# Kernel tuning notes

Hardware: AMD Instinct MI355X
Metric: run time of the kernel (lower is better)

## Reference

```python
import jax, jax.numpy as jnp
import numpy as np

B, S, ENC, DEC, ATTN = 32, 4096, 512, 512, 512


def setup_inputs() -> dict:
    key = jax.random.key(0)
    k1, k2, k3, k4, k5, k6 = jax.random.split(key, 6)
    h = jax.random.normal(k1, (B, DEC), dtype=jnp.float32)
    enc_out = jax.random.normal(k2, (B, S, ENC), dtype=jnp.float32)
    mask = jax.random.randint(k3, (B, S), 0, 2).astype(bool)
    # torch nn.Linear(in, out, bias=False): y = x @ W.T with W [out, in].
    # Store weights as [in, out] so y = x @ W; same math.
    sc = 1.0 / np.sqrt(DEC)
    W_h = jax.random.normal(k4, (DEC, ATTN), dtype=jnp.float32) * sc
    W_s = jax.random.normal(k5, (ENC, ATTN), dtype=jnp.float32) * sc
    v = jax.random.normal(k6, (ATTN,), dtype=jnp.float32) * sc
    return {"h": h, "enc_out": enc_out, "mask": mask, "W_h": W_h, "W_s": W_s, "v": v}


def reference(h, enc_out, mask, W_h, W_s, v):
    # query: [B, 1, A]; key: [B, S, A]
    query = (h @ W_h)[:, None, :]
    key = jnp.einsum("bse,ea->bsa", enc_out, W_s)
    energy = jnp.tanh(query + key)                    # [B, S, A]
    score = jnp.einsum("bsa,a->bs", energy, v)        # v^T tanh(...)
    score = jnp.where(mask, jnp.float32(-1e9), score)
    attn = jax.nn.softmax(score, axis=-1)             # [B, S]
    ctx = jnp.einsum("bs,bse->be", attn, enc_out)     # weighted sum
    return (ctx, attn)
```

## Files before the change

kernel.cpp:

```cpp
#include <hip/hip_runtime.h>
#include <hip/hip_bf16.h>
#include <math.h>

#define BB 32
#define SS 4096
#define EE 512
#define AA 512

typedef short bf16x8 __attribute__((ext_vector_type(8)));
typedef float f32x4 __attribute__((ext_vector_type(4)));
typedef unsigned short u16x4 __attribute__((ext_vector_type(4)));

__device__ __forceinline__ unsigned short f2bf(float f) {
  unsigned int u = __float_as_uint(f);
  u += 0x7fffu + ((u >> 16) & 1u);
  return (unsigned short)(u >> 16);
}

__device__ __forceinline__ float bf2f(unsigned short s) {
  return __uint_as_float(((unsigned int)s) << 16);
}

__device__ __forceinline__ float tanh_fast(float x) {
  return 1.f - 2.f / (__expf(2.f * x) + 1.f);
}

__global__ void query_kernel(const float* __restrict__ h,
                             const float* __restrict__ Wh,
                             float* __restrict__ q) {
  __shared__ float hrow[EE];
  int b = blockIdx.x;
  int t = threadIdx.x;
  for (int i = t; i < EE; i += 256) hrow[i] = h[b * EE + i];
  __syncthreads();
  float a0 = 0.f, a1 = 0.f;
  for (int e = 0; e < EE; ++e) {
    float hv = hrow[e];
    a0 += hv * Wh[e * AA + t];
    a1 += hv * Wh[e * AA + t + 256];
  }
  q[b * AA + t] = a0;
  q[b * AA + t + 256] = a1;
}

__global__ void wst_kernel(const float* __restrict__ Ws,
                           unsigned short* __restrict__ Wst) {
  int i = blockIdx.x * 256 + threadIdx.x;
  int a = i >> 9, e = i & 511;
  Wst[a * EE + e] = f2bf(Ws[e * AA + a]);
}

__global__ __launch_bounds__(256, 2) void fused_kernel(
    const float* __restrict__ enc, const unsigned short* __restrict__ Wst,
    const float* __restrict__ q, const float* __restrict__ v,
    const int* __restrict__ mask,
    float* __restrict__ rawscore,
    float* __restrict__ ctxp,
    float* __restrict__ mbuf) {
  __shared__ __align__(16) unsigned short Atile[64 * 512];
  __shared__ float spart[4][64];
  __shared__ float wrow[64];
  __shared__ float pbuf[4][512];
  const int b = blockIdx.y, chunk = blockIdx.x;
  const int s0 = chunk * 64;
  const int tid = threadIdx.x;

  const float4* src = (const float4*)(enc + ((size_t)b * SS + s0) * EE);
  for (int pass = 0; pass < 2; ++pass) {
#pragma unroll
    for (int i = 0; i < 16; ++i) {
      int idx = (pass * 16 + i) * 256 + tid;
      float4 x = src[idx];
      int row = idx >> 7;
      int c4 = idx & 127;
      int ch = c4 >> 1;
      int within = (c4 & 1) * 4;
      int cs = ch ^ (row & 7);
      u16x4 p;
      p.x = f2bf(x.x); p.y = f2bf(x.y); p.z = f2bf(x.z); p.w = f2bf(x.w);
      *(u16x4*)&Atile[row * 512 + cs * 8 + within] = p;
    }
  }
  __syncthreads();

  const int w = tid >> 6, lane = tid & 63;
  const int quad = lane >> 4, l16 = lane & 15;

  float srow[4][4];
#pragma unroll
  for (int m = 0; m < 4; ++m)
#pragma unroll
    for (int r = 0; r < 4; ++r) srow[m][r] = 0.f;

  for (int h = 0; h < 2; ++h) {
    const int n0 = w * 128 + h * 64;
    f32x4 acc[4][4];
#pragma unroll
    for (int m = 0; m < 4; ++m)
#pragma unroll
      for (int n = 0; n < 4; ++n) acc[m][n] = (f32x4){0.f, 0.f, 0.f, 0.f};

    const unsigned short* wb = Wst + (size_t)(n0 + l16) * EE + quad * 8;
#pragma unroll 2
    for (int k0 = 0; k0 < 512; k0 += 32) {
      int cs = ((k0 >> 3) + quad) ^ (l16 & 7);
      bf16x8 aF[4], bF[4];
#pragma unroll
      for (int m = 0; m < 4; ++m)
        aF[m] = *(const bf16x8*)&Atile[(m * 16 + l16) * 512 + cs * 8];
#pragma unroll
      for (int n = 0; n < 4; ++n)
        bF[n] = *(const bf16x8*)&wb[(size_t)n * 16 * EE + k0];
#pragma unroll
      for (int m = 0; m < 4; ++m)
#pragma unroll
        for (int n = 0; n < 4; ++n)
          acc[m][n] =
              __builtin_amdgcn_mfma_f32_16x16x32_bf16(aF[m], bF[n], acc[m][n], 0, 0, 0);
    }
#pragma unroll
    for (int n = 0; n < 4; ++n) {
      float qn = q[b * AA + n0 + n * 16 + l16];
      float vn = v[n0 + n * 16 + l16];
#pragma unroll
      for (int m = 0; m < 4; ++m)
#pragma unroll
        for (int r = 0; r < 4; ++r)
          srow[m][r] += tanh_fast(qn + acc[m][n][r]) * vn;
    }
  }

#pragma unroll
  for (int m = 0; m < 4; ++m)
#pragma unroll
    for (int r = 0; r < 4; ++r) {
      float s = srow[m][r];
      s += __shfl_xor(s, 1, 64);
      s += __shfl_xor(s, 2, 64);
      s += __shfl_xor(s, 4, 64);
      s += __shfl_xor(s, 8, 64);
      if (l16 == 0) spart[w][m * 16 + quad * 4 + r] = s;
    }
  __syncthreads();

  if (tid < 64) {
    float raw = spart[0][tid] + spart[1][tid] + spart[2][tid] + spart[3][tid];
    float sc = mask[(size_t)b * SS + s0 + tid] ? -1e9f : raw;
    rawscore[(size_t)b * SS + s0 + tid] = sc;
    float mx = sc;
    for (int off = 1; off < 64; off <<= 1)
      mx = fmaxf(mx, __shfl_xor(mx, off, 64));
    wrow[tid] = __expf(sc - mx);
    if (tid == 0) mbuf[b * 64 + chunk] = mx;
  }
  __syncthreads();

  {
    const int c = tid & 63;
    const int sg = tid >> 6;
    float a8[8] = {0.f, 0.f, 0.f, 0.f, 0.f, 0.f, 0.f, 0.f};
#pragma unroll
    for (int i = 0; i < 16; ++i) {
      int row = sg * 16 + i;
      float wgt = wrow[row];
      bf16x8 av = *(const bf16x8*)&Atile[row * 512 + ((c ^ (row & 7)) * 8)];
#pragma unroll
      for (int j = 0; j < 8; ++j)
        a8[j] += wgt * bf2f((unsigned short)av[j]);
    }
#pragma unroll
    for (int j = 0; j < 8; ++j) pbuf[sg][c * 8 + j] = a8[j];
  }
  __syncthreads();
#pragma unroll
  for (int jj = 0; jj < 2; ++jj) {
    int e = jj * 256 + tid;
    ctxp[((size_t)b * 64 + chunk) * EE + e] =
        pbuf[0][e] + pbuf[1][e] + pbuf[2][e] + pbuf[3][e];
  }
}

__global__ void finalize_kernel(float* __restrict__ attn,
                                const float* __restrict__ ctxp,
                                const float* __restrict__ mbuf,
                                float* __restrict__ ctx) {
  __shared__ float red[8];
  __shared__ float fc[64];
  int b = blockIdx.x, t = threadIdx.x;
  float* row = attn + (size_t)b * SS;
  float vals[16];
  float m = -3e38f;
#pragma unroll
  for (int i = 0; i < 16; ++i) {
    float x = row[i * 256 + t];
    vals[i] = x;
    m = fmaxf(m, x);
  }
  for (int off = 1; off < 64; off <<= 1) m = fmaxf(m, __shfl_xor(m, off, 64));
  int wv = t >> 6, ln = t & 63;
  if (ln == 0) red[wv] = m;
  __syncthreads();
  m = fmaxf(fmaxf(red[0], red[1]), fmaxf(red[2], red[3]));
  float sum = 0.f;
#pragma unroll
  for (int i = 0; i < 16; ++i) { vals[i] = __expf(vals[i] - m); sum += vals[i]; }
  for (int off = 1; off < 64; off <<= 1) sum += __shfl_xor(sum, off, 64);
  if (ln == 0) red[4 + wv] = sum;
  __syncthreads();
  sum = red[4] + red[5] + red[6] + red[7];
  float inv = 1.f / sum;
#pragma unroll
  for (int i = 0; i < 16; ++i) row[i * 256 + t] = vals[i] * inv;

  if (t < 64) fc[t] = __expf(mbuf[b * 64 + t] - m) * inv;
  __syncthreads();
#pragma unroll
  for (int jj = 0; jj < 2; ++jj) {
    int e = jj * 256 + t;
    const float* p = ctxp + (size_t)b * 64 * EE + e;
    float s = 0.f;
#pragma unroll
    for (int c = 0; c < 64; ++c) s += fc[c] * p[c * EE];
    ctx[b * EE + e] = s;
  }
}

extern "C" void kernel_launch(void* const* d_in, const int* in_sizes, int n_in,
                              void* d_out, int out_size, void* d_ws, size_t ws_size,
                              hipStream_t stream) {
  const float* h    = (const float*)d_in[0];
  const float* enc  = (const float*)d_in[1];
  const int*   mask = (const int*)d_in[2];
  const float* Wh   = (const float*)d_in[3];
  const float* Ws   = (const float*)d_in[4];
  const float* v    = (const float*)d_in[5];

  float* out  = (float*)d_out;
  float* ctx  = out;
  float* attn = out + BB * EE;

  char* ws = (char*)d_ws;
  float* qws = (float*)ws;                         ws += (size_t)BB * AA * 4;
  unsigned short* Wst = (unsigned short*)ws;       ws += (size_t)AA * EE * 2;
  float* ctxp = (float*)ws;                        ws += (size_t)BB * 64 * EE * 4;
  float* mbuf = (float*)ws;

  hipLaunchKernelGGL(query_kernel, dim3(32), dim3(256), 0, stream, h, Wh, qws);
  hipLaunchKernelGGL(wst_kernel, dim3(1024), dim3(256), 0, stream, Ws, Wst);
  hipLaunchKernelGGL(fused_kernel, dim3(SS / 64, BB), dim3(256), 0, stream,
                     enc, Wst, qws, v, mask, attn, ctxp, mbuf);
  hipLaunchKernelGGL(finalize_kernel, dim3(BB), dim3(256), 0, stream,
                     attn, ctxp, mbuf, ctx);
}
```

Before: 540.9 us.

## Pipeline encoder tile loads with MFMA, widen blocks to 512 threads, tile Ws transpose

The fused kernel now uses 512 threads, with each wave owning 64 attention columns. It streams the encoder tile in eight 64-column chunks, using register double buffering so global loads overlap MFMA work on the chunk already staged. The ctx partial reduction becomes one thread per feature with no pbuf scratch. The Ws transpose uses a shared-memory tile for coalesced access, and finalize moves to 512 threads. The trade-offs are a barrier per chunk, more register pressure from the 4-blocks-per-CU launch bound, and a 64KB LDS tile that may limit how many blocks actually fit per CU.

Measured after the change: 529.9 us. 1.02x faster.

```diff
diff --git a/kernel.cpp b/kernel.cpp
--- a/kernel.cpp
+++ b/kernel.cpp
@@ -45,12 +45,24 @@
 
 __global__ void wst_kernel(const float* __restrict__ Ws,
                            unsigned short* __restrict__ Wst) {
-  int i = blockIdx.x * 256 + threadIdx.x;
-  int a = i >> 9, e = i & 511;
-  Wst[a * EE + e] = f2bf(Ws[e * AA + a]);
-}
-
-__global__ __launch_bounds__(256, 2) void fused_kernel(
+  __shared__ unsigned short tile[64][65];
+  const int a0 = blockIdx.x * 64, e0 = blockIdx.y * 64;
+  const int t = threadIdx.x;
+  const int c = t & 63, r0 = t >> 6;
+#pragma unroll
+  for (int i = 0; i < 16; ++i) {
+    int e = r0 + i * 4;
+    tile[c][e] = f2bf(Ws[(size_t)(e0 + e) * AA + a0 + c]);
+  }
+  __syncthreads();
+#pragma unroll
+  for (int i = 0; i < 16; ++i) {
+    int a = r0 + i * 4;
+    Wst[(size_t)(a0 + a) * EE + e0 + c] = tile[a][c];
+  }
+}
+
+__global__ __launch_bounds__(512, 4) void fused_kernel(
     const float* __restrict__ enc, const unsigned short* __restrict__ Wst,
     const float* __restrict__ q, const float* __restrict__ v,
     const int* __restrict__ mask,
@@ -58,78 +70,91 @@
     float* __restrict__ ctxp,
     float* __restrict__ mbuf) {
   __shared__ __align__(16) unsigned short Atile[64 * 512];
-  __shared__ float spart[4][64];
+  __shared__ float spart[8][64];
   __shared__ float wrow[64];
-  __shared__ float pbuf[4][512];
   const int b = blockIdx.y, chunk = blockIdx.x;
   const int s0 = chunk * 64;
   const int tid = threadIdx.x;
-
-  const float4* src = (const float4*)(enc + ((size_t)b * SS + s0) * EE);
-  for (int pass = 0; pass < 2; ++pass) {
-#pragma unroll
-    for (int i = 0; i < 16; ++i) {
-      int idx = (pass * 16 + i) * 256 + tid;
-      float4 x = src[idx];
-      int row = idx >> 7;
-      int c4 = idx & 127;
-      int ch = c4 >> 1;
-      int within = (c4 & 1) * 4;
-      int cs = ch ^ (row & 7);
+  const int w = tid >> 6, lane = tid & 63;
+  const int quad = lane >> 4, l16 = lane & 15;
+  const int n0 = w * 64;
+
+  const int rbase = tid >> 4;
+  const int c4 = tid & 15;
+  const int sw3 = (rbase & 7) << 3;
+  const float4* src4 = (const float4*)(enc + ((size_t)b * SS + s0) * EE);
+  const float4* g0 = src4 + rbase * 128 + c4;
+  const float4* g1 = g0 + 32 * 128;
+  unsigned short* st0 = &Atile[rbase * 512 + ((c4 * 4) ^ sw3)];
+  unsigned short* st1 = st0 + 32 * 512;
+
+  const unsigned short* wb = Wst + (size_t)(n0 + l16) * EE + quad * 8;
+
+  f32x4 acc[4][4];
+#pragma unroll
+  for (int m = 0; m < 4; ++m)
+#pragma unroll
+    for (int j = 0; j < 4; ++j) acc[m][j] = (f32x4){0.f, 0.f, 0.f, 0.f};
+
+  float4 rb[2][2];
+  rb[0][0] = g0[0];
+  rb[0][1] = g1[0];
+
+#pragma unroll
+  for (int c = 0; c < 8; ++c) {
+    const int cur = c & 1, nxt = cur ^ 1;
+    {
+      float4 x = rb[cur][0];
       u16x4 p;
       p.x = f2bf(x.x); p.y = f2bf(x.y); p.z = f2bf(x.z); p.w = f2bf(x.w);
-      *(u16x4*)&Atile[row * 512 + cs * 8 + within] = p;
-    }
-  }
-  __syncthreads();
-
-  const int w = tid >> 6, lane = tid & 63;
-  const int quad = lane >> 4, l16 = lane & 15;
+      *(u16x4*)(st0 + c * 64) = p;
+      float4 y = rb[cur][1];
+      u16x4 p2;
+      p2.x = f2bf(y.x); p2.y = f2bf(y.y); p2.z = f2bf(y.z); p2.w = f2bf(y.w);
+      *(u16x4*)(st1 + c * 64) = p2;
+    }
+    if (c < 7) {
+      rb[nxt][0] = g0[(c + 1) * 16];
+      rb[nxt][1] = g1[(c + 1) * 16];
+    }
+    asm volatile("s_waitcnt lgkmcnt(0)" ::: "memory");
+    __builtin_amdgcn_s_barrier();
+#pragma unroll
+    for (int kk = 0; kk < 2; ++kk) {
+      const int k0 = c * 64 + kk * 32;
+      bf16x8 aF[4];
+#pragma unroll
+      for (int m = 0; m < 4; ++m) {
+        const int row = m * 16 + l16;
+        aF[m] = *(const bf16x8*)&Atile[row * 512 +
+                                       ((k0 + quad * 8) ^ ((row & 7) << 3))];
+      }
+#pragma unroll
+      for (int j = 0; j < 4; ++j) {
+        bf16x8 bF = *(const bf16x8*)&wb[(size_t)j * 16 * EE + k0];
+#pragma unroll
+        for (int m = 0; m < 4; ++m)
+          acc[m][j] = __builtin_amdgcn_mfma_f32_16x16x32_bf16(aF[m], bF,
+                                                              acc[m][j], 0, 0, 0);
+      }
+    }
+  }
 
   float srow[4][4];
 #pragma unroll
   for (int m = 0; m < 4; ++m)
 #pragma unroll
     for (int r = 0; r < 4; ++r) srow[m][r] = 0.f;
-
-  for (int h = 0; h < 2; ++h) {
-    const int n0 = w * 128 + h * 64;
-    f32x4 acc[4][4];
+#pragma unroll
+  for (int j = 0; j < 4; ++j) {
+    float qn = q[b * AA + n0 + j * 16 + l16];
+    float vn = v[n0 + j * 16 + l16];
 #pragma unroll
     for (int m = 0; m < 4; ++m)
 #pragma unroll
-      for (int n = 0; n < 4; ++n) acc[m][n] = (f32x4){0.f, 0.f, 0.f, 0.f};
-
-    const unsigned short* wb = Wst + (size_t)(n0 + l16) * EE + quad * 8;
-#pragma unroll 2
-    for (int k0 = 0; k0 < 512; k0 += 32) {
-      int cs = ((k0 >> 3) + quad) ^ (l16 & 7);
-      bf16x8 aF[4], bF[4];
-#pragma unroll
-      for (int m = 0; m < 4; ++m)
-        aF[m] = *(const bf16x8*)&Atile[(m * 16 + l16) * 512 + cs * 8];
-#pragma unroll
-      for (int n = 0; n < 4; ++n)
-        bF[n] = *(const bf16x8*)&wb[(size_t)n * 16 * EE + k0];
-#pragma unroll
-      for (int m = 0; m < 4; ++m)
-#pragma unroll
-        for (int n = 0; n < 4; ++n)
-          acc[m][n] =
-              __builtin_amdgcn_mfma_f32_16x16x32_bf16(aF[m], bF[n], acc[m][n], 0, 0, 0);
-    }
-#pragma unroll
-    for (int n = 0; n < 4; ++n) {
-      float qn = q[b * AA + n0 + n * 16 + l16];
-      float vn = v[n0 + n * 16 + l16];
-#pragma unroll
-      for (int m = 0; m < 4; ++m)
-#pragma unroll
-        for (int r = 0; r < 4; ++r)
-          srow[m][r] += tanh_fast(qn + acc[m][n][r]) * vn;
-    }
-  }
-
+      for (int r = 0; r < 4; ++r)
+        srow[m][r] += tanh_fast(qn + acc[m][j][r]) * vn;
+  }
 #pragma unroll
   for (int m = 0; m < 4; ++m)
 #pragma unroll
@@ -144,7 +169,9 @@
   __syncthreads();
 
   if (tid < 64) {
-    float raw = spart[0][tid] + spart[1][tid] + spart[2][tid] + spart[3][tid];
+    float raw = 0.f;
+#pragma unroll
+    for (int ww = 0; ww < 8; ++ww) raw += spart[ww][tid];
     float sc = mask[(size_t)b * SS + s0 + tid] ? -1e9f : raw;
     rawscore[(size_t)b * SS + s0 + tid] = sc;
     float mx = sc;
@@ -156,43 +183,27 @@
   __syncthreads();
 
   {
-    const int c = tid & 63;
-    const int sg = tid >> 6;
-    float a8[8] = {0.f, 0.f, 0.f, 0.f, 0.f, 0.f, 0.f, 0.f};
-#pragma unroll
-    for (int i = 0; i < 16; ++i) {
-      int row = sg * 16 + i;
-      float wgt = wrow[row];
-      bf16x8 av = *(const bf16x8*)&Atile[row * 512 + ((c ^ (row & 7)) * 8)];
-#pragma unroll
-      for (int j = 0; j < 8; ++j)
-        a8[j] += wgt * bf2f((unsigned short)av[j]);
-    }
-#pragma unroll
-    for (int j = 0; j < 8; ++j) pbuf[sg][c * 8 + j] = a8[j];
-  }
-  __syncthreads();
-#pragma unroll
-  for (int jj = 0; jj < 2; ++jj) {
-    int e = jj * 256 + tid;
-    ctxp[((size_t)b * 64 + chunk) * EE + e] =
-        pbuf[0][e] + pbuf[1][e] + pbuf[2][e] + pbuf[3][e];
-  }
-}
-
-__global__ void finalize_kernel(float* __restrict__ attn,
-                                const float* __restrict__ ctxp,
-                                const float* __restrict__ mbuf,
-                                float* __restrict__ ctx) {
-  __shared__ float red[8];
+    const int e = tid;
+    float a = 0.f;
+#pragma unroll 8
+    for (int row = 0; row < 64; ++row)
+      a += wrow[row] * bf2f(Atile[row * 512 + (e ^ ((row & 7) << 3))]);
+    ctxp[((size_t)b * 64 + chunk) * EE + e] = a;
+  }
+}
+
+__global__ __launch_bounds__(512) void finalize_kernel(
+    float* __restrict__ attn, const float* __restrict__ ctxp,
+    const float* __restrict__ mbuf, float* __restrict__ ctx) {
+  __shared__ float red[16];
   __shared__ float fc[64];
   int b = blockIdx.x, t = threadIdx.x;
   float* row = attn + (size_t)b * SS;
-  float vals[16];
+  float vals[8];
   float m = -3e38f;
 #pragma unroll
-  for (int i = 0; i < 16; ++i) {
-    float x = row[i * 256 + t];
+  for (int i = 0; i < 8; ++i) {
+    float x = row[i * 512 + t];
     vals[i] = x;
     m = fmaxf(m, x);
   }
@@ -200,28 +211,30 @@
   int wv = t >> 6, ln = t & 63;
   if (ln == 0) red[wv] = m;
   __syncthreads();
-  m = fmaxf(fmaxf(red[0], red[1]), fmaxf(red[2], red[3]));
+  m = red[0];
+#pragma unroll
+  for (int i = 1; i < 8; ++i) m = fmaxf(m, red[i]);
   float sum = 0.f;
 #pragma unroll
-  for (int i = 0; i < 16; ++i) { vals[i] = __expf(vals[i] - m); sum += vals[i]; }
+  for (int i = 0; i < 8; ++i) { vals[i] = __expf(vals[i] - m); sum += vals[i]; }
   for (int off = 1; off < 64; off <<= 1) sum += __shfl_xor(sum, off, 64);
-  if (ln == 0) red[4 + wv] = sum;
-  __syncthreads();
-  sum = red[4] + red[5] + red[6] + red[7];
+  if (ln == 0) red[8 + wv] = sum;
+  __syncthreads();
+  sum = 0.f;
+#pragma unroll
+  for (int i = 0; i < 8; ++i) sum += red[8 + i];
   float inv = 1.f / sum;
 #pragma unroll
-  for (int i = 0; i < 16; ++i) row[i * 256 + t] = vals[i] * inv;
+  for (int i = 0; i < 8; ++i) row[i * 512 + t] = vals[i] * inv;
 
   if (t < 64) fc[t] = __expf(mbuf[b * 64 + t] - m) * inv;
   __syncthreads();
-#pragma unroll
-  for (int jj = 0; jj < 2; ++jj) {
-    int e = jj * 256 + t;
-    const float* p = ctxp + (size_t)b * 64 * EE + e;
+  {
+    const float* p = ctxp + (size_t)b * 64 * EE + t;
     float s = 0.f;
 #pragma unroll
     for (int c = 0; c < 64; ++c) s += fc[c] * p[c * EE];
-    ctx[b * EE + e] = s;
+    ctx[b * EE + t] = s;
   }
 }
 
@@ -246,9 +259,9 @@
   float* mbuf = (float*)ws;
 
   hipLaunchKernelGGL(query_kernel, dim3(32), dim3(256), 0, stream, h, Wh, qws);
-  hipLaunchKernelGGL(wst_kernel, dim3(1024), dim3(256), 0, stream, Ws, Wst);
-  hipLaunchKernelGGL(fused_kernel, dim3(SS / 64, BB), dim3(256), 0, stream,
+  hipLaunchKernelGGL(wst_kernel, dim3(8, 8), dim3(256), 0, stream, Ws, Wst);
+  hipLaunchKernelGGL(fused_kernel, dim3(SS / 64, BB), dim3(512), 0, stream,
                      enc, Wst, qws, v, mask, attn, ctxp, mbuf);
-  hipLaunchKernelGGL(finalize_kernel, dim3(BB), dim3(256), 0, stream,
+  hipLaunchKernelGGL(finalize_kernel, dim3(BB), dim3(512), 0, stream,
                      attn, ctxp, mbuf, ctx);
 }
```
